# Performance work log

Measured on AMD Instinct MI355X. Metric: run time of the kernel, lower is better.

Reference implementation:

```python
import jax, jax.numpy as jnp
import numpy as np


def setup_inputs() -> dict:
    key = jax.random.key(0)
    k1, k2, k3, k4 = jax.random.split(key, 4)
    B, T, M = 4, 2048, 1024   # batch, seq, d_model -> S = 8192 tokens
    E, F = 16, 4096           # experts (world_size*num_local_experts), d_ff
    x = jax.random.normal(k1, (B, T, M), dtype=jnp.float32) * 0.02
    Wg = jax.random.normal(k2, (M, E), dtype=jnp.float32) * 0.02
    w1 = jax.random.normal(k3, (E, M, F), dtype=jnp.float32) * 0.02
    w2 = jax.random.normal(k4, (E, F, M), dtype=jnp.float32) * 0.02
    return {"x": x, "Wg": Wg, "w1": w1, "w2": w2}


def reference(x, Wg, w1, w2):
    d = x.shape[-1]
    xr = x.reshape(-1, d)                     # (S, M)
    S = xr.shape[0]
    E = Wg.shape[1]
    C = (S + E - 1) // E                      # capacity (capacity_factor = 1.0)

    # top-1 gating (gate module = linear + softmax)
    gate = jax.nn.softmax(xr @ Wg, axis=-1)   # (S, E)
    idx = jnp.argmax(gate, axis=1)            # (S,) expert index per token
    gates_s = jnp.take_along_axis(gate, idx[:, None], axis=1)[:, 0]  # (S,)

    # cumulative-sum location within chosen expert
    onehot = jax.nn.one_hot(idx, E, dtype=jnp.int32)           # (S, E)
    loc = jnp.sum((jnp.cumsum(onehot, axis=0) - 1) * onehot, axis=1)  # (S,)
    valid = loc < C                                             # capacity drop mask

    # scatter dispatch: overflow tokens routed to a pad slot C, then sliced off
    loc_pad = jnp.minimum(loc, C)
    dispatched = jnp.zeros((E, C + 1, d), dtype=x.dtype).at[idx, loc_pad].set(xr)
    dispatched = dispatched[:, :C]            # (E, C, M)

    # all-to-all is identity (FakeAllToAllOp); per-expert FFN
    h = jax.nn.relu(jnp.einsum('ecm,emf->ecf', dispatched, w1))   # (E, C, F)
    expert_out = jnp.einsum('ecf,efm->ecm', h, w2)                # (E, C, M)

    # gather combine: rout[i] = gate_s[i] * expert_out[idx[i], loc[i]] if loc < C
    gathered = expert_out[idx, jnp.minimum(loc, C - 1)]           # (S, M)
    combined = gathered * (gates_s * valid.astype(x.dtype))[:, None]
    return combined.reshape(x.shape)
```

## Files before the change

### kernel.cpp

```cpp
#include <hip/hip_runtime.h>
#include <cstdint>
#include <cstddef>

#define S_TOK 8192
#define DM    1024
#define NE    16
#define NF    4096
#define CAP   512

typedef __attribute__((ext_vector_type(8))) short bf16x8;
typedef __attribute__((ext_vector_type(4))) float f32x4;

__device__ __forceinline__ unsigned short f2bf(float f) {
  __bf16 b = (__bf16)f;
  return __builtin_bit_cast(unsigned short, b);
}
__device__ __forceinline__ unsigned pk2(float a, float b) {
  return (unsigned)f2bf(a) | ((unsigned)f2bf(b) << 16);
}
__device__ __forceinline__ int pcol(int c) { return c ^ ((c >> 3) & 7); }

__device__ __forceinline__ void gload_lds16(const void* g, void* l) {
  __builtin_amdgcn_global_load_lds(
      (const __attribute__((address_space(1))) void*)g,
      (__attribute__((address_space(3))) void*)l, 16, 0, 0);
}

__global__ void __launch_bounds__(256)
zero_kernel(float4* __restrict__ Out, int n4) {
  const int stride = gridDim.x * 256;
  for (int i = blockIdx.x * 256 + threadIdx.x; i < n4; i += stride)
    Out[i] = float4{0.f, 0.f, 0.f, 0.f};
}

__global__ void __launch_bounds__(256)
gate_kernel(const float* __restrict__ X, const float* __restrict__ Wg,
            int* __restrict__ idx, float* __restrict__ gval) {
  const int tid  = threadIdx.x;
  const int lane = tid & 63;
  const int wid  = tid >> 6;
  const int e = lane & 15, q = lane >> 4;
  const int t0 = blockIdx.x * 16 + wid * 4;
  const int mbase = q * 256;

  const float* xp0 = X + (size_t)(t0 + 0) * DM + mbase;
  const float* xp1 = X + (size_t)(t0 + 1) * DM + mbase;
  const float* xp2 = X + (size_t)(t0 + 2) * DM + mbase;
  const float* xp3 = X + (size_t)(t0 + 3) * DM + mbase;
  const float* wp  = Wg + (size_t)mbase * NE + e;

  float a0 = 0.f, a1 = 0.f, a2 = 0.f, a3 = 0.f;
#pragma unroll 4
  for (int i = 0; i < 64; ++i) {
    float4 x0 = *(const float4*)(xp0 + i * 4);
    float4 x1 = *(const float4*)(xp1 + i * 4);
    float4 x2 = *(const float4*)(xp2 + i * 4);
    float4 x3 = *(const float4*)(xp3 + i * 4);
    float w0 = wp[(i * 4 + 0) * NE];
    float w1 = wp[(i * 4 + 1) * NE];
    float w2 = wp[(i * 4 + 2) * NE];
    float w3 = wp[(i * 4 + 3) * NE];
    a0 = fmaf(x0.x, w0, fmaf(x0.y, w1, fmaf(x0.z, w2, fmaf(x0.w, w3, a0))));
    a1 = fmaf(x1.x, w0, fmaf(x1.y, w1, fmaf(x1.z, w2, fmaf(x1.w, w3, a1))));
    a2 = fmaf(x2.x, w0, fmaf(x2.y, w1, fmaf(x2.z, w2, fmaf(x2.w, w3, a2))));
    a3 = fmaf(x3.x, w0, fmaf(x3.y, w1, fmaf(x3.z, w2, fmaf(x3.w, w3, a3))));
  }
#pragma unroll
  for (int s = 16; s < 64; s <<= 1) {
    a0 += __shfl_xor(a0, s, 64);
    a1 += __shfl_xor(a1, s, 64);
    a2 += __shfl_xor(a2, s, 64);
    a3 += __shfl_xor(a3, s, 64);
  }
  float l = (q == 0) ? a0 : (q == 1) ? a1 : (q == 2) ? a2 : a3;
  float bv = l; int bi = e;
#pragma unroll
  for (int s = 1; s < 16; s <<= 1) {
    float ov = __shfl_xor(bv, s, 16);
    int   oi = __shfl_xor(bi, s, 16);
    if (ov > bv || (ov == bv && oi < bi)) { bv = ov; bi = oi; }
  }
  float p  = expf(l - bv);
  float sm = p;
#pragma unroll
  for (int s = 1; s < 16; s <<= 1) sm += __shfl_xor(sm, s, 16);
  if (e == 0) {
    idx[t0 + q]  = bi;
    gval[t0 + q] = 1.0f / sm;
  }
}

__global__ void __launch_bounds__(1024)
scan_kernel(const int* __restrict__ idx, int* __restrict__ s2t) {
  const int tid = threadIdx.x;
#pragma unroll
  for (int k = 0; k < 8; ++k) s2t[tid + k * 1024] = -1;
  __shared__ int base[16];
  __shared__ int wavecnt[16][16];
  if (tid < 16) base[tid] = 0;
  __syncthreads();
  const int wid = tid >> 6, lane = tid & 63;
  const unsigned long long ltmask = (1ull << lane) - 1ull;
  for (int c = 0; c < 8; ++c) {
    const int t = c * 1024 + tid;
    const int e = idx[t];
    int rank = 0;
#pragma unroll
    for (int ee = 0; ee < 16; ++ee) {
      unsigned long long m = __ballot(e == ee);
      if (lane == 0) wavecnt[wid][ee] = __popcll(m);
      if (ee == e) rank = __popcll(m & ltmask);
    }
    __syncthreads();
    if (tid < 16) {
      int s = base[tid];
#pragma unroll
      for (int w = 0; w < 16; ++w) { int cc = wavecnt[w][tid]; wavecnt[w][tid] = s; s += cc; }
      base[tid] = s;
    }
    __syncthreads();
    const int loc = wavecnt[wid][e] + rank;
    if (loc < CAP) s2t[e * CAP + loc] = t;
    __syncthreads();
  }
}

__global__ void __launch_bounds__(256)
gather_kernel(const float* __restrict__ X, const int* __restrict__ s2t,
              unsigned short* __restrict__ Xg) {
  const int tid = threadIdx.x;
  const int d  = tid & 127;
  const int sl = tid >> 7;
  const int s0 = blockIdx.x * 16;
#pragma unroll 2
  for (int p = 0; p < 8; ++p) {
    const int s = s0 + p * 2 + sl;
    const int tok = s2t[s];
    uint4 w;
    if (tok >= 0) {
      const float* xp = X + (size_t)tok * DM + d * 8;
      float4 v0 = *(const float4*)xp;
      float4 v1 = *(const float4*)(xp + 4);
      w = make_uint4(pk2(v0.x, v0.y), pk2(v0.z, v0.w),
                     pk2(v1.x, v1.y), pk2(v1.z, v1.w));
    } else {
      w = make_uint4(0u, 0u, 0u, 0u);
    }
    char* dst = (char*)Xg + (size_t)(s >> 9) * 1048576 +
                (size_t)(d >> 3) * 65536 + (size_t)(d & 7) * 8192 +
                (size_t)(s & 511) * 16;
    *(uint4*)dst = w;
  }
}



#define G1_BX 4
#define G1_BY 32
#define G1_BZ 16
__global__ void __launch_bounds__(256, 2)
gemm1_kernel(const unsigned short* __restrict__ Xg, const float* __restrict__ W1,
             unsigned short* __restrict__ H2) {
  constexpr int NT = DM / 64;
  __shared__ __align__(16) char lds[81920];

  const int tid = threadIdx.x;
  const int lane = tid & 63, wid = tid >> 6;
  const int wr = wid >> 1, wc = wid & 1;
  const int ln15 = lane & 15, l16 = lane >> 4;

  const int flat = blockIdx.x + G1_BX * (blockIdx.y + G1_BY * blockIdx.z);
  const int xcd = flat & 7, jj = flat >> 3;
  const int e  = xcd * 2 + (jj >> 7);
  const int rr = jj & 127;
  const int by = rr >> 2, bx = rr & 3;
  const int m0 = bx * 128, n0 = by * 128;

  char* const Bb0 = lds + 49152;
  char* const Bb1 = lds + 65536;

  const int rb = wid >> 1;
  const int kgw = (wid & 1) * 4;
  const int adst = kgw * 2048 + rb * 1024;
  const char* const Xge = (const char*)Xg + (size_t)e * 1048576 +
                          (size_t)(m0 + rb * 64 + lane) * 16;

  const int c0 = (tid & 31) * 4;
  const int kq = tid >> 5;
  const float* const bsrc = W1 + (size_t)e * DM * NF + (size_t)(kq * 8) * NF + n0 + c0;
  int bwoff[4];
#pragma unroll
  for (int cc = 0; cc < 4; ++cc) bwoff[cc] = kq * 2048 + pcol(c0 + cc) * 16;

  int aoff[4], boff[4];
#pragma unroll
  for (int mi = 0; mi < 4; ++mi)
    aoff[mi] = l16 * 2048 + wr * 1024 + (mi * 16 + ln15) * 16;
#pragma unroll
  for (int ni = 0; ni < 4; ++ni)
    boff[ni] = l16 * 2048 + pcol(wc * 64 + ni * 16 + ln15) * 16;

  f32x4 acc[4][4];
#pragma unroll
  for (int mi = 0; mi < 4; ++mi)
#pragma unroll
    for (int ni = 0; ni < 4; ++ni) acc[mi][ni] = f32x4{0.f, 0.f, 0.f, 0.f};

  float4 breg[8];

  auto ISSUE_B = [&](int kt) {
    const float* bp = bsrc + (size_t)kt * 64 * NF;
#pragma unroll
    for (int r = 0; r < 8; ++r) breg[r] = *(const float4*)(bp + (size_t)r * NF);
  };
  auto ISSUE_A = [&](int Aoff, int kt) {
#pragma unroll
    for (int j = 0; j < 4; ++j)
      gload_lds16(Xge + (size_t)kt * 65536 + (size_t)(kgw + j) * 8192,
                  lds + Aoff + adst + j * 2048);
  };
  auto WRITEB = [&](char* Bbuf) {
    const float* f = (const float*)breg;
#pragma unroll
    for (int cc = 0; cc < 4; ++cc)
      *(uint4*)(Bbuf + bwoff[cc]) =
          make_uint4(pk2(f[0 * 4 + cc], f[1 * 4 + cc]), pk2(f[2 * 4 + cc], f[3 * 4 + cc]),
                     pk2(f[4 * 4 + cc], f[5 * 4 + cc]), pk2(f[6 * 4 + cc], f[7 * 4 + cc]));
  };
  auto COMPUTE = [&](int Aoff, const char* Bbuf) {
#pragma unroll
    for (int kk = 0; kk < 2; ++kk) {
      bf16x8 af[4], bf[4];
#pragma unroll
      for (int mi = 0; mi < 4; ++mi)
        af[mi] = *(const bf16x8*)(lds + Aoff + kk * 8192 + aoff[mi]);
#pragma unroll
      for (int ni = 0; ni < 4; ++ni)
        bf[ni] = *(const bf16x8*)(Bbuf + kk * 8192 + boff[ni]);
#pragma unroll
      for (int mi = 0; mi < 4; ++mi)
#pragma unroll
        for (int ni = 0; ni < 4; ++ni)
          acc[mi][ni] = __builtin_amdgcn_mfma_f32_16x16x32_bf16(af[mi], bf[ni], acc[mi][ni], 0, 0, 0);
    }
  };

  ISSUE_B(0); ISSUE_A(0, 0);
  WRITEB(Bb0);
  ISSUE_B(1); ISSUE_A(16384, 1);
  asm volatile("s_waitcnt vmcnt(12) lgkmcnt(0)" ::: "memory");
  __builtin_amdgcn_s_barrier();

  int aCur = 0, aNxt = 16384, aNx2 = 32768;
  for (int kt = 0; kt < NT; ++kt) {
    WRITEB((kt & 1) ? Bb0 : Bb1);
    const int tl = (kt + 2 < NT) ? kt + 2 : NT - 1;
    ISSUE_B(tl);
    ISSUE_A(aNx2, tl);
    COMPUTE(aCur, (kt & 1) ? Bb1 : Bb0);
    asm volatile("s_waitcnt vmcnt(12) lgkmcnt(0)" ::: "memory");
    __builtin_amdgcn_s_barrier();
    const int t = aCur; aCur = aNxt; aNxt = aNx2; aNx2 = t;
  }
  asm volatile("s_waitcnt vmcnt(0)" ::: "memory");
  __builtin_amdgcn_s_barrier();

  char* img = lds;
#pragma unroll
  for (int mi = 0; mi < 4; ++mi) {
#pragma unroll
    for (int ni = 0; ni < 4; ++ni) {
      const int colL = wc * 64 + ni * 16 + ln15;
      const int basei = (colL >> 6) * 16384 + ((colL >> 3) & 7) * 2048 + (colL & 7) * 2;
#pragma unroll
      for (int j = 0; j < 4; ++j) {
        const int rowL = wr * 64 + mi * 16 + l16 * 4 + j;
        float v = acc[mi][ni][j];
        v = v > 0.f ? v : 0.f;
        *(unsigned short*)(img + basei + rowL * 16) = f2bf(v);
      }
    }
  }
  __syncthreads();
  const char* src = img + tid * 128;
  char* dst = (char*)H2 + (size_t)e * 4194304 +
              (size_t)((n0 >> 6) + (tid >> 7)) * 65536 +
              (size_t)((tid >> 4) & 7) * 8192 +
              (size_t)(m0 + (tid & 15) * 8) * 16;
#pragma unroll
  for (int u = 0; u < 8; ++u)
    *(uint4*)(dst + u * 16) = *(const uint4*)(src + u * 16);
}

#define G2_BX 4
#define G2_BY 8
#define G2_BZ 16
__global__ void __launch_bounds__(256, 2)
gemm2_kernel(const unsigned short* __restrict__ H2, const float* __restrict__ W2,
             const int* __restrict__ s2t, const float* __restrict__ gval,
             float* __restrict__ Out) {
  constexpr int NT = NF / 64;
  __shared__ __align__(16) char lds[81920];

  const int tid = threadIdx.x;
  const int lane = tid & 63, wid = tid >> 6;
  const int wr = wid >> 1, wc = wid & 1;
  const int ln15 = lane & 15, l16 = lane >> 4;

  const int flat = blockIdx.x + G2_BX * (blockIdx.y + G2_BY * blockIdx.z);
  const int xcd = flat & 7, jj = flat >> 3;
  const int e  = xcd * 2 + (jj >> 5);
  const int rr = jj & 31;
  const int by = rr >> 2, bx = rr & 3;
  const int m0 = bx * 128, n0 = by * 128;

  char* const Bb0 = lds + 49152;
  char* const Bb1 = lds + 65536;

  const int rb = wid >> 1;
  const int kgw = (wid & 1) * 4;
  const int adst = kgw * 2048 + rb * 1024;
  const char* const Hex = (const char*)H2 + (size_t)e * 4194304 +
                          (size_t)(m0 + rb * 64 + lane) * 16;

  const int c0 = (tid & 31) * 4;
  const int kq = tid >> 5;
  const float* const bsrc = W2 + (size_t)e * NF * DM + (size_t)(kq * 8) * DM + n0 + c0;
  int bwoff[4];
#pragma unroll
  for (int cc = 0; cc < 4; ++cc) bwoff[cc] = kq * 2048 + pcol(c0 + cc) * 16;

  int aoff[4], boff[4];
#pragma unroll
  for (int mi = 0; mi < 4; ++mi)
    aoff[mi] = l16 * 2048 + wr * 1024 + (mi * 16 + ln15) * 16;
#pragma unroll
  for (int ni = 0; ni < 4; ++ni)
    boff[ni] = l16 * 2048 + pcol(wc * 64 + ni * 16 + ln15) * 16;

  f32x4 acc[4][4];
#pragma unroll
  for (int mi = 0; mi < 4; ++mi)
#pragma unroll
    for (int ni = 0; ni < 4; ++ni) acc[mi][ni] = f32x4{0.f, 0.f, 0.f, 0.f};

  float4 breg[8];

  auto ISSUE_B = [&](int kt) {
    const float* bp = bsrc + (size_t)kt * 64 * DM;
#pragma unroll
    for (int r = 0; r < 8; ++r) breg[r] = *(const float4*)(bp + (size_t)r * DM);
  };
  auto ISSUE_A = [&](int Aoff, int kt) {
#pragma unroll
    for (int j = 0; j < 4; ++j)
      gload_lds16(Hex + (size_t)kt * 65536 + (size_t)(kgw + j) * 8192,
                  lds + Aoff + adst + j * 2048);
  };
  auto WRITEB = [&](char* Bbuf) {
    const float* f = (const float*)breg;
#pragma unroll
    for (int cc = 0; cc < 4; ++cc)
      *(uint4*)(Bbuf + bwoff[cc]) =
          make_uint4(pk2(f[0 * 4 + cc], f[1 * 4 + cc]), pk2(f[2 * 4 + cc], f[3 * 4 + cc]),
                     pk2(f[4 * 4 + cc], f[5 * 4 + cc]), pk2(f[6 * 4 + cc], f[7 * 4 + cc]));
  };
  auto COMPUTE = [&](int Aoff, const char* Bbuf) {
#pragma unroll
    for (int kk = 0; kk < 2; ++kk) {
      bf16x8 af[4], bf[4];
#pragma unroll
      for (int mi = 0; mi < 4; ++mi)
        af[mi] = *(const bf16x8*)(lds + Aoff + kk * 8192 + aoff[mi]);
#pragma unroll
      for (int ni = 0; ni < 4; ++ni)
        bf[ni] = *(const bf16x8*)(Bbuf + kk * 8192 + boff[ni]);
#pragma unroll
      for (int mi = 0; mi < 4; ++mi)
#pragma unroll
        for (int ni = 0; ni < 4; ++ni)
          acc[mi][ni] = __builtin_amdgcn_mfma_f32_16x16x32_bf16(af[mi], bf[ni], acc[mi][ni], 0, 0, 0);
    }
  };

  ISSUE_B(0); ISSUE_A(0, 0);
  WRITEB(Bb0);
  ISSUE_B(1); ISSUE_A(16384, 1);
  asm volatile("s_waitcnt vmcnt(12) lgkmcnt(0)" ::: "memory");
  __builtin_amdgcn_s_barrier();

  int aCur = 0, aNxt = 16384, aNx2 = 32768;
  for (int kt = 0; kt < NT; ++kt) {
    WRITEB((kt & 1) ? Bb0 : Bb1);
    const int tl = (kt + 2 < NT) ? kt + 2 : NT - 1;
    ISSUE_B(tl);
    ISSUE_A(aNx2, tl);
    COMPUTE(aCur, (kt & 1) ? Bb1 : Bb0);
    asm volatile("s_waitcnt vmcnt(12) lgkmcnt(0)" ::: "memory");
    __builtin_amdgcn_s_barrier();
    const int t = aCur; aCur = aNxt; aNxt = aNx2; aNx2 = t;
  }
  asm volatile("s_waitcnt vmcnt(0)" ::: "memory");

#pragma unroll
  for (int mi = 0; mi < 4; ++mi) {
#pragma unroll
    for (int ni = 0; ni < 4; ++ni) {
      const int col = n0 + wc * 64 + ni * 16 + ln15;
#pragma unroll
      for (int j = 0; j < 4; ++j) {
        const int row = m0 + wr * 64 + mi * 16 + l16 * 4 + j;
        const int tk = s2t[e * CAP + row];
        if (tk >= 0)
          Out[(size_t)tk * DM + col] = acc[mi][ni][j] * gval[tk];
      }
    }
  }
}

extern "C" void kernel_launch(void* const* d_in, const int* in_sizes, int n_in,
                              void* d_out, int out_size, void* d_ws, size_t ws_size,
                              hipStream_t stream) {
  (void)in_sizes; (void)n_in; (void)ws_size;
  const float* X  = (const float*)d_in[0];
  const float* Wg = (const float*)d_in[1];
  const float* W1 = (const float*)d_in[2];
  const float* W2 = (const float*)d_in[3];
  float* Out = (float*)d_out;

  char* ws = (char*)d_ws;
  int*   s2t  = (int*)ws;
  int*   idx  = (int*)(ws + 32768);
  float* gval = (float*)(ws + 65536);
  unsigned short* Xg = (unsigned short*)(ws + 98304);
  unsigned short* H2 = (unsigned short*)(ws + 98304 + 16777216);

  zero_kernel<<<2048, 256, 0, stream>>>((float4*)Out, out_size / 4);
  gate_kernel<<<S_TOK / 16, 256, 0, stream>>>(X, Wg, idx, gval);
  scan_kernel<<<1, 1024, 0, stream>>>(idx, s2t);
  gather_kernel<<<512, 256, 0, stream>>>(X, s2t, Xg);
  gemm1_kernel<<<dim3(G1_BX, G1_BY, G1_BZ), 256, 0, stream>>>(Xg, W1, H2);
  gemm2_kernel<<<dim3(G2_BX, G2_BY, G2_BZ), 256, 0, stream>>>(H2, W2, s2t, gval, Out);
}
```

Baseline: 301.2 us.

## Split GEMM tiles across eight waves and deepen B register prefetch

Both expert GEMM kernels move from 256 to 512 threads per block while keeping the 128x128 output tile. Each wave now computes 32x64 instead of 64x64, which halves the accumulators and per-thread global loads and roughly doubles the resident waves per CU to hide memory latency. The B operand is now held in two alternating register buffers, with the loop unrolled by two, so fp32 weight loads are issued one more tile ahead. The cost is more barrier participants, more address overhead per useful MFMA, and lower per-wave operand reuse from LDS.

New measurement: 312.4 us. 3.7% more time.

```diff
diff --git a/kernel.cpp b/kernel.cpp
--- a/kernel.cpp
+++ b/kernel.cpp
@@ -158,7 +158,7 @@
 #define G1_BX 4
 #define G1_BY 32
 #define G1_BZ 16
-__global__ void __launch_bounds__(256, 2)
+__global__ void __launch_bounds__(512, 4)
 gemm1_kernel(const unsigned short* __restrict__ Xg, const float* __restrict__ W1,
              unsigned short* __restrict__ H2) {
   constexpr int NT = DM / 64;
@@ -179,102 +179,109 @@
   char* const Bb0 = lds + 49152;
   char* const Bb1 = lds + 65536;
 
-  const int rb = wid >> 1;
-  const int kgw = (wid & 1) * 4;
-  const int adst = kgw * 2048 + rb * 1024;
-  const char* const Xge = (const char*)Xg + (size_t)e * 1048576 +
-                          (size_t)(m0 + rb * 64 + lane) * 16;
+  const char* const aSrc = (const char*)Xg + (size_t)e * 1048576 +
+                           (size_t)(m0 + (wid & 1) * 64 + lane) * 16;
+  const int adst = (wid >> 1) * 2048 + (wid & 1) * 1024;
 
   const int c0 = (tid & 31) * 4;
   const int kq = tid >> 5;
-  const float* const bsrc = W1 + (size_t)e * DM * NF + (size_t)(kq * 8) * NF + n0 + c0;
+  const float* const bsrc = W1 + (size_t)e * DM * NF + (size_t)(kq * 4) * NF + n0 + c0;
   int bwoff[4];
 #pragma unroll
-  for (int cc = 0; cc < 4; ++cc) bwoff[cc] = kq * 2048 + pcol(c0 + cc) * 16;
-
-  int aoff[4], boff[4];
-#pragma unroll
-  for (int mi = 0; mi < 4; ++mi)
-    aoff[mi] = l16 * 2048 + wr * 1024 + (mi * 16 + ln15) * 16;
+  for (int cc = 0; cc < 4; ++cc)
+    bwoff[cc] = (kq >> 1) * 2048 + pcol(c0 + cc) * 16 + (kq & 1) * 8;
+
+  int aoff[2], boff[4];
+#pragma unroll
+  for (int mi = 0; mi < 2; ++mi)
+    aoff[mi] = l16 * 2048 + (wr * 32 + mi * 16 + ln15) * 16;
 #pragma unroll
   for (int ni = 0; ni < 4; ++ni)
     boff[ni] = l16 * 2048 + pcol(wc * 64 + ni * 16 + ln15) * 16;
 
-  f32x4 acc[4][4];
-#pragma unroll
-  for (int mi = 0; mi < 4; ++mi)
+  f32x4 acc[2][4];
+#pragma unroll
+  for (int mi = 0; mi < 2; ++mi)
 #pragma unroll
     for (int ni = 0; ni < 4; ++ni) acc[mi][ni] = f32x4{0.f, 0.f, 0.f, 0.f};
 
-  float4 breg[8];
-
-  auto ISSUE_B = [&](int kt) {
+  float4 bA[4], bB[4];
+
+  auto ISSUE_B = [&](float4* br, int kt) {
     const float* bp = bsrc + (size_t)kt * 64 * NF;
 #pragma unroll
-    for (int r = 0; r < 8; ++r) breg[r] = *(const float4*)(bp + (size_t)r * NF);
+    for (int r = 0; r < 4; ++r) br[r] = *(const float4*)(bp + (size_t)r * NF);
   };
   auto ISSUE_A = [&](int Aoff, int kt) {
-#pragma unroll
-    for (int j = 0; j < 4; ++j)
-      gload_lds16(Xge + (size_t)kt * 65536 + (size_t)(kgw + j) * 8192,
-                  lds + Aoff + adst + j * 2048);
-  };
-  auto WRITEB = [&](char* Bbuf) {
-    const float* f = (const float*)breg;
+    gload_lds16(aSrc + (size_t)kt * 65536 + (size_t)(wid >> 1) * 8192,
+                lds + Aoff + adst);
+    gload_lds16(aSrc + (size_t)kt * 65536 + (size_t)((wid >> 1) + 4) * 8192,
+                lds + Aoff + adst + 8192);
+  };
+  auto WRITEB = [&](char* Bbuf, const float4* br) {
+    const float* f = (const float*)br;
 #pragma unroll
     for (int cc = 0; cc < 4; ++cc)
-      *(uint4*)(Bbuf + bwoff[cc]) =
-          make_uint4(pk2(f[0 * 4 + cc], f[1 * 4 + cc]), pk2(f[2 * 4 + cc], f[3 * 4 + cc]),
-                     pk2(f[4 * 4 + cc], f[5 * 4 + cc]), pk2(f[6 * 4 + cc], f[7 * 4 + cc]));
+      *(uint2*)(Bbuf + bwoff[cc]) =
+          make_uint2(pk2(f[0 * 4 + cc], f[1 * 4 + cc]),
+                     pk2(f[2 * 4 + cc], f[3 * 4 + cc]));
   };
   auto COMPUTE = [&](int Aoff, const char* Bbuf) {
 #pragma unroll
     for (int kk = 0; kk < 2; ++kk) {
-      bf16x8 af[4], bf[4];
-#pragma unroll
-      for (int mi = 0; mi < 4; ++mi)
+      bf16x8 af[2], bf[4];
+#pragma unroll
+      for (int mi = 0; mi < 2; ++mi)
         af[mi] = *(const bf16x8*)(lds + Aoff + kk * 8192 + aoff[mi]);
 #pragma unroll
       for (int ni = 0; ni < 4; ++ni)
         bf[ni] = *(const bf16x8*)(Bbuf + kk * 8192 + boff[ni]);
 #pragma unroll
-      for (int mi = 0; mi < 4; ++mi)
+      for (int mi = 0; mi < 2; ++mi)
 #pragma unroll
         for (int ni = 0; ni < 4; ++ni)
           acc[mi][ni] = __builtin_amdgcn_mfma_f32_16x16x32_bf16(af[mi], bf[ni], acc[mi][ni], 0, 0, 0);
     }
   };
 
-  ISSUE_B(0); ISSUE_A(0, 0);
-  WRITEB(Bb0);
-  ISSUE_B(1); ISSUE_A(16384, 1);
-  asm volatile("s_waitcnt vmcnt(12) lgkmcnt(0)" ::: "memory");
+  ISSUE_B(bA, 0); ISSUE_A(0, 0);
+  WRITEB(Bb0, bA);
+  ISSUE_B(bB, 1); ISSUE_A(16384, 1);
+  ISSUE_B(bA, 2);
+  asm volatile("s_waitcnt vmcnt(10) lgkmcnt(0)" ::: "memory");
   __builtin_amdgcn_s_barrier();
 
   int aCur = 0, aNxt = 16384, aNx2 = 32768;
-  for (int kt = 0; kt < NT; ++kt) {
-    WRITEB((kt & 1) ? Bb0 : Bb1);
-    const int tl = (kt + 2 < NT) ? kt + 2 : NT - 1;
-    ISSUE_B(tl);
-    ISSUE_A(aNx2, tl);
-    COMPUTE(aCur, (kt & 1) ? Bb1 : Bb0);
-    asm volatile("s_waitcnt vmcnt(12) lgkmcnt(0)" ::: "memory");
+#pragma unroll 1
+  for (int kt = 0; kt < NT; kt += 2) {
+    WRITEB(Bb1, bB);
+    ISSUE_B(bB, (kt + 3 < NT) ? kt + 3 : NT - 1);
+    ISSUE_A(aNx2, (kt + 2 < NT) ? kt + 2 : NT - 1);
+    COMPUTE(aCur, Bb0);
+    asm volatile("s_waitcnt vmcnt(6) lgkmcnt(0)" ::: "memory");
     __builtin_amdgcn_s_barrier();
-    const int t = aCur; aCur = aNxt; aNxt = aNx2; aNx2 = t;
+    int t = aCur; aCur = aNxt; aNxt = aNx2; aNx2 = t;
+    WRITEB(Bb0, bA);
+    ISSUE_B(bA, (kt + 4 < NT) ? kt + 4 : NT - 1);
+    ISSUE_A(aNx2, (kt + 3 < NT) ? kt + 3 : NT - 1);
+    COMPUTE(aCur, Bb1);
+    asm volatile("s_waitcnt vmcnt(6) lgkmcnt(0)" ::: "memory");
+    __builtin_amdgcn_s_barrier();
+    t = aCur; aCur = aNxt; aNxt = aNx2; aNx2 = t;
   }
   asm volatile("s_waitcnt vmcnt(0)" ::: "memory");
   __builtin_amdgcn_s_barrier();
 
   char* img = lds;
 #pragma unroll
-  for (int mi = 0; mi < 4; ++mi) {
+  for (int mi = 0; mi < 2; ++mi) {
 #pragma unroll
     for (int ni = 0; ni < 4; ++ni) {
       const int colL = wc * 64 + ni * 16 + ln15;
       const int basei = (colL >> 6) * 16384 + ((colL >> 3) & 7) * 2048 + (colL & 7) * 2;
 #pragma unroll
       for (int j = 0; j < 4; ++j) {
-        const int rowL = wr * 64 + mi * 16 + l16 * 4 + j;
+        const int rowL = wr * 32 + mi * 16 + l16 * 4 + j;
         float v = acc[mi][ni][j];
         v = v > 0.f ? v : 0.f;
         *(unsigned short*)(img + basei + rowL * 16) = f2bf(v);
@@ -282,20 +289,20 @@
     }
   }
   __syncthreads();
-  const char* src = img + tid * 128;
+  const char* src = img + tid * 64;
   char* dst = (char*)H2 + (size_t)e * 4194304 +
-              (size_t)((n0 >> 6) + (tid >> 7)) * 65536 +
-              (size_t)((tid >> 4) & 7) * 8192 +
-              (size_t)(m0 + (tid & 15) * 8) * 16;
-#pragma unroll
-  for (int u = 0; u < 8; ++u)
+              (size_t)((n0 >> 6) + (tid >> 8)) * 65536 +
+              (size_t)((tid >> 5) & 7) * 8192 +
+              (size_t)(m0 + ((tid * 4) & 127)) * 16;
+#pragma unroll
+  for (int u = 0; u < 4; ++u)
     *(uint4*)(dst + u * 16) = *(const uint4*)(src + u * 16);
 }
 
 #define G2_BX 4
 #define G2_BY 8
 #define G2_BZ 16
-__global__ void __launch_bounds__(256, 2)
+__global__ void __launch_bounds__(512, 4)
 gemm2_kernel(const unsigned short* __restrict__ H2, const float* __restrict__ W2,
              const int* __restrict__ s2t, const float* __restrict__ gval,
              float* __restrict__ Out) {
@@ -317,99 +324,106 @@
   char* const Bb0 = lds + 49152;
   char* const Bb1 = lds + 65536;
 
-  const int rb = wid >> 1;
-  const int kgw = (wid & 1) * 4;
-  const int adst = kgw * 2048 + rb * 1024;
-  const char* const Hex = (const char*)H2 + (size_t)e * 4194304 +
-                          (size_t)(m0 + rb * 64 + lane) * 16;
+  const char* const aSrc = (const char*)H2 + (size_t)e * 4194304 +
+                           (size_t)(m0 + (wid & 1) * 64 + lane) * 16;
+  const int adst = (wid >> 1) * 2048 + (wid & 1) * 1024;
 
   const int c0 = (tid & 31) * 4;
   const int kq = tid >> 5;
-  const float* const bsrc = W2 + (size_t)e * NF * DM + (size_t)(kq * 8) * DM + n0 + c0;
+  const float* const bsrc = W2 + (size_t)e * NF * DM + (size_t)(kq * 4) * DM + n0 + c0;
   int bwoff[4];
 #pragma unroll
-  for (int cc = 0; cc < 4; ++cc) bwoff[cc] = kq * 2048 + pcol(c0 + cc) * 16;
-
-  int aoff[4], boff[4];
-#pragma unroll
-  for (int mi = 0; mi < 4; ++mi)
-    aoff[mi] = l16 * 2048 + wr * 1024 + (mi * 16 + ln15) * 16;
+  for (int cc = 0; cc < 4; ++cc)
+    bwoff[cc] = (kq >> 1) * 2048 + pcol(c0 + cc) * 16 + (kq & 1) * 8;
+
+  int aoff[2], boff[4];
+#pragma unroll
+  for (int mi = 0; mi < 2; ++mi)
+    aoff[mi] = l16 * 2048 + (wr * 32 + mi * 16 + ln15) * 16;
 #pragma unroll
   for (int ni = 0; ni < 4; ++ni)
     boff[ni] = l16 * 2048 + pcol(wc * 64 + ni * 16 + ln15) * 16;
 
-  f32x4 acc[4][4];
-#pragma unroll
-  for (int mi = 0; mi < 4; ++mi)
+  f32x4 acc[2][4];
+#pragma unroll
+  for (int mi = 0; mi < 2; ++mi)
 #pragma unroll
     for (int ni = 0; ni < 4; ++ni) acc[mi][ni] = f32x4{0.f, 0.f, 0.f, 0.f};
 
-  float4 breg[8];
-
-  auto ISSUE_B = [&](int kt) {
+  float4 bA[4], bB[4];
+
+  auto ISSUE_B = [&](float4* br, int kt) {
     const float* bp = bsrc + (size_t)kt * 64 * DM;
 #pragma unroll
-    for (int r = 0; r < 8; ++r) breg[r] = *(const float4*)(bp + (size_t)r * DM);
+    for (int r = 0; r < 4; ++r) br[r] = *(const float4*)(bp + (size_t)r * DM);
   };
   auto ISSUE_A = [&](int Aoff, int kt) {
-#pragma unroll
-    for (int j = 0; j < 4; ++j)
-      gload_lds16(Hex + (size_t)kt * 65536 + (size_t)(kgw + j) * 8192,
-                  lds + Aoff + adst + j * 2048);
-  };
-  auto WRITEB = [&](char* Bbuf) {
-    const float* f = (const float*)breg;
+    gload_lds16(aSrc + (size_t)kt * 65536 + (size_t)(wid >> 1) * 8192,
+                lds + Aoff + adst);
+    gload_lds16(aSrc + (size_t)kt * 65536 + (size_t)((wid >> 1) + 4) * 8192,
+                lds + Aoff + adst + 8192);
+  };
+  auto WRITEB = [&](char* Bbuf, const float4* br) {
+    const float* f = (const float*)br;
 #pragma unroll
     for (int cc = 0; cc < 4; ++cc)
-      *(uint4*)(Bbuf + bwoff[cc]) =
-          make_uint4(pk2(f[0 * 4 + cc], f[1 * 4 + cc]), pk2(f[2 * 4 + cc], f[3 * 4 + cc]),
-                     pk2(f[4 * 4 + cc], f[5 * 4 + cc]), pk2(f[6 * 4 + cc], f[7 * 4 + cc]));
+      *(uint2*)(Bbuf + bwoff[cc]) =
+          make_uint2(pk2(f[0 * 4 + cc], f[1 * 4 + cc]),
+                     pk2(f[2 * 4 + cc], f[3 * 4 + cc]));
   };
   auto COMPUTE = [&](int Aoff, const char* Bbuf) {
 #pragma unroll
     for (int kk = 0; kk < 2; ++kk) {
-      bf16x8 af[4], bf[4];
-#pragma unroll
-      for (int mi = 0; mi < 4; ++mi)
+      bf16x8 af[2], bf[4];
+#pragma unroll
+      for (int mi = 0; mi < 2; ++mi)
         af[mi] = *(const bf16x8*)(lds + Aoff + kk * 8192 + aoff[mi]);
 #pragma unroll
       for (int ni = 0; ni < 4; ++ni)
         bf[ni] = *(const bf16x8*)(Bbuf + kk * 8192 + boff[ni]);
 #pragma unroll
-      for (int mi = 0; mi < 4; ++mi)
+      for (int mi = 0; mi < 2; ++mi)
 #pragma unroll
         for (int ni = 0; ni < 4; ++ni)
           acc[mi][ni] = __builtin_amdgcn_mfma_f32_16x16x32_bf16(af[mi], bf[ni], acc[mi][ni], 0, 0, 0);
     }
   };
 
-  ISSUE_B(0); ISSUE_A(0, 0);
-  WRITEB(Bb0);
-  ISSUE_B(1); ISSUE_A(16384, 1);
-  asm volatile("s_waitcnt vmcnt(12) lgkmcnt(0)" ::: "memory");
+  ISSUE_B(bA, 0); ISSUE_A(0, 0);
+  WRITEB(Bb0, bA);
+  ISSUE_B(bB, 1); ISSUE_A(16384, 1);
+  ISSUE_B(bA, 2);
+  asm volatile("s_waitcnt vmcnt(10) lgkmcnt(0)" ::: "memory");
   __builtin_amdgcn_s_barrier();
 
   int aCur = 0, aNxt = 16384, aNx2 = 32768;
-  for (int kt = 0; kt < NT; ++kt) {
-    WRITEB((kt & 1) ? Bb0 : Bb1);
-    const int tl = (kt + 2 < NT) ? kt + 2 : NT - 1;
-    ISSUE_B(tl);
-    ISSUE_A(aNx2, tl);
-    COMPUTE(aCur, (kt & 1) ? Bb1 : Bb0);
-    asm volatile("s_waitcnt vmcnt(12) lgkmcnt(0)" ::: "memory");
+#pragma unroll 1
+  for (int kt = 0; kt < NT; kt += 2) {
+    WRITEB(Bb1, bB);
+    ISSUE_B(bB, (kt + 3 < NT) ? kt + 3 : NT - 1);
+    ISSUE_A(aNx2, (kt + 2 < NT) ? kt + 2 : NT - 1);
+    COMPUTE(aCur, Bb0);
+    asm volatile("s_waitcnt vmcnt(6) lgkmcnt(0)" ::: "memory");
     __builtin_amdgcn_s_barrier();
-    const int t = aCur; aCur = aNxt; aNxt = aNx2; aNx2 = t;
+    int t = aCur; aCur = aNxt; aNxt = aNx2; aNx2 = t;
+    WRITEB(Bb0, bA);
+    ISSUE_B(bA, (kt + 4 < NT) ? kt + 4 : NT - 1);
+    ISSUE_A(aNx2, (kt + 3 < NT) ? kt + 3 : NT - 1);
+    COMPUTE(aCur, Bb1);
+    asm volatile("s_waitcnt vmcnt(6) lgkmcnt(0)" ::: "memory");
+    __builtin_amdgcn_s_barrier();
+    t = aCur; aCur = aNxt; aNxt = aNx2; aNx2 = t;
   }
   asm volatile("s_waitcnt vmcnt(0)" ::: "memory");
 
 #pragma unroll
-  for (int mi = 0; mi < 4; ++mi) {
+  for (int mi = 0; mi < 2; ++mi) {
 #pragma unroll
     for (int ni = 0; ni < 4; ++ni) {
       const int col = n0 + wc * 64 + ni * 16 + ln15;
 #pragma unroll
       for (int j = 0; j < 4; ++j) {
-        const int row = m0 + wr * 64 + mi * 16 + l16 * 4 + j;
+        const int row = m0 + wr * 32 + mi * 16 + l16 * 4 + j;
         const int tk = s2t[e * CAP + row];
         if (tk >= 0)
           Out[(size_t)tk * DM + col] = acc[mi][ni][j] * gval[tk];
@@ -439,6 +453,6 @@
   gate_kernel<<<S_TOK / 16, 256, 0, stream>>>(X, Wg, idx, gval);
   scan_kernel<<<1, 1024, 0, stream>>>(idx, s2t);
   gather_kernel<<<512, 256, 0, stream>>>(X, s2t, Xg);
-  gemm1_kernel<<<dim3(G1_BX, G1_BY, G1_BZ), 256, 0, stream>>>(Xg, W1, H2);
-  gemm2_kernel<<<dim3(G2_BX, G2_BY, G2_BZ), 256, 0, stream>>>(H2, W2, s2t, gval, Out);
-}
+  gemm1_kernel<<<dim3(G1_BX, G1_BY, G1_BZ), 512, 0, stream>>>(Xg, W1, H2);
+  gemm2_kernel<<<dim3(G2_BX, G2_BY, G2_BZ), 512, 0, stream>>>(H2, W2, s2t, gval, Out);
+}
```

## Restructure GEMM pipelines with register double-buffered B and smaller LDS for occupancy

Applied to the files above, without the earlier changes.

Both expert GEMM kernels drop from 80KB to 48KB of LDS. They now use a single B tile in LDS and double-buffer the fp32 B loads in registers (bP/bQ), with two A buffers alternated in an unrolled-by-2 loop. Launch bounds rise to 3 blocks per CU, and MFMA sections are wrapped in s_setprio to favour matrix issue. The extra register buffer and the added barriers per iteration may raise register pressure and cause spills at the higher occupancy target. Wrapped (kt+N)&NTM prefetches issue redundant loads at the tail.

After: 1.001 ms. 3.32x slower.

```diff
diff --git a/kernel.cpp b/kernel.cpp
--- a/kernel.cpp
+++ b/kernel.cpp
@@ -158,11 +158,12 @@
 #define G1_BX 4
 #define G1_BY 32
 #define G1_BZ 16
-__global__ void __launch_bounds__(256, 2)
+__global__ void __launch_bounds__(256, 3)
 gemm1_kernel(const unsigned short* __restrict__ Xg, const float* __restrict__ W1,
              unsigned short* __restrict__ H2) {
   constexpr int NT = DM / 64;
-  __shared__ __align__(16) char lds[81920];
+  constexpr int NTM = NT - 1;
+  __shared__ __align__(16) char lds[49152];
 
   const int tid = threadIdx.x;
   const int lane = tid & 63, wid = tid >> 6;
@@ -176,29 +177,28 @@
   const int by = rr >> 2, bx = rr & 3;
   const int m0 = bx * 128, n0 = by * 128;
 
-  char* const Bb0 = lds + 49152;
-  char* const Bb1 = lds + 65536;
+  char* const Bs = lds + 32768;
 
   const int rb = wid >> 1;
   const int kgw = (wid & 1) * 4;
   const int adst = kgw * 2048 + rb * 1024;
-  const char* const Xge = (const char*)Xg + (size_t)e * 1048576 +
-                          (size_t)(m0 + rb * 64 + lane) * 16;
+  const char* const aSrc = (const char*)Xg + (size_t)e * 1048576 +
+                           (size_t)(m0 + rb * 64 + lane) * 16;
 
   const int c0 = (tid & 31) * 4;
   const int kq = tid >> 5;
   const float* const bsrc = W1 + (size_t)e * DM * NF + (size_t)(kq * 8) * NF + n0 + c0;
   int bwoff[4];
 #pragma unroll
-  for (int cc = 0; cc < 4; ++cc) bwoff[cc] = kq * 2048 + pcol(c0 + cc) * 16;
+  for (int cc = 0; cc < 4; ++cc) bwoff[cc] = 32768 + kq * 2048 + pcol(c0 + cc) * 16;
 
   int aoff[4], boff[4];
 #pragma unroll
   for (int mi = 0; mi < 4; ++mi)
-    aoff[mi] = l16 * 2048 + wr * 1024 + (mi * 16 + ln15) * 16;
+    aoff[mi] = l16 * 2048 + (wr * 64 + mi * 16 + ln15) * 16;
 #pragma unroll
   for (int ni = 0; ni < 4; ++ni)
-    boff[ni] = l16 * 2048 + pcol(wc * 64 + ni * 16 + ln15) * 16;
+    boff[ni] = 32768 + l16 * 2048 + pcol(wc * 64 + ni * 16 + ln15) * 16;
 
   f32x4 acc[4][4];
 #pragma unroll
@@ -206,28 +206,28 @@
 #pragma unroll
     for (int ni = 0; ni < 4; ++ni) acc[mi][ni] = f32x4{0.f, 0.f, 0.f, 0.f};
 
-  float4 breg[8];
-
-  auto ISSUE_B = [&](int kt) {
+  float4 bP[8], bQ[8];
+
+  auto ISSUE_B = [&](float4* br, int kt) {
     const float* bp = bsrc + (size_t)kt * 64 * NF;
 #pragma unroll
-    for (int r = 0; r < 8; ++r) breg[r] = *(const float4*)(bp + (size_t)r * NF);
+    for (int r = 0; r < 8; ++r) br[r] = *(const float4*)(bp + (size_t)r * NF);
   };
   auto ISSUE_A = [&](int Aoff, int kt) {
 #pragma unroll
     for (int j = 0; j < 4; ++j)
-      gload_lds16(Xge + (size_t)kt * 65536 + (size_t)(kgw + j) * 8192,
+      gload_lds16(aSrc + (size_t)kt * 65536 + (size_t)(kgw + j) * 8192,
                   lds + Aoff + adst + j * 2048);
   };
-  auto WRITEB = [&](char* Bbuf) {
-    const float* f = (const float*)breg;
+  auto WRITEB = [&](const float4* br) {
+    const float* f = (const float*)br;
 #pragma unroll
     for (int cc = 0; cc < 4; ++cc)
-      *(uint4*)(Bbuf + bwoff[cc]) =
+      *(uint4*)(lds + bwoff[cc]) =
           make_uint4(pk2(f[0 * 4 + cc], f[1 * 4 + cc]), pk2(f[2 * 4 + cc], f[3 * 4 + cc]),
                      pk2(f[4 * 4 + cc], f[5 * 4 + cc]), pk2(f[6 * 4 + cc], f[7 * 4 + cc]));
   };
-  auto COMPUTE = [&](int Aoff, const char* Bbuf) {
+  auto COMPUTE = [&](int Aoff) {
 #pragma unroll
     for (int kk = 0; kk < 2; ++kk) {
       bf16x8 af[4], bf[4];
@@ -236,31 +236,40 @@
         af[mi] = *(const bf16x8*)(lds + Aoff + kk * 8192 + aoff[mi]);
 #pragma unroll
       for (int ni = 0; ni < 4; ++ni)
-        bf[ni] = *(const bf16x8*)(Bbuf + kk * 8192 + boff[ni]);
+        bf[ni] = *(const bf16x8*)(lds + kk * 8192 + boff[ni]);
+      __builtin_amdgcn_s_setprio(1);
 #pragma unroll
       for (int mi = 0; mi < 4; ++mi)
 #pragma unroll
         for (int ni = 0; ni < 4; ++ni)
           acc[mi][ni] = __builtin_amdgcn_mfma_f32_16x16x32_bf16(af[mi], bf[ni], acc[mi][ni], 0, 0, 0);
-    }
-  };
-
-  ISSUE_B(0); ISSUE_A(0, 0);
-  WRITEB(Bb0);
-  ISSUE_B(1); ISSUE_A(16384, 1);
-  asm volatile("s_waitcnt vmcnt(12) lgkmcnt(0)" ::: "memory");
+      __builtin_amdgcn_s_setprio(0);
+    }
+  };
+
+  ISSUE_B(bP, 0);  ISSUE_A(0, 0);
+  ISSUE_B(bQ, 1);  ISSUE_A(16384, 1);
+  WRITEB(bP);
+  ISSUE_B(bP, 2);
+  asm volatile("s_waitcnt vmcnt(20) lgkmcnt(0)" ::: "memory");
   __builtin_amdgcn_s_barrier();
 
-  int aCur = 0, aNxt = 16384, aNx2 = 32768;
-  for (int kt = 0; kt < NT; ++kt) {
-    WRITEB((kt & 1) ? Bb0 : Bb1);
-    const int tl = (kt + 2 < NT) ? kt + 2 : NT - 1;
-    ISSUE_B(tl);
-    ISSUE_A(aNx2, tl);
-    COMPUTE(aCur, (kt & 1) ? Bb1 : Bb0);
+#pragma unroll 1
+  for (int kt = 0; kt < NT; kt += 2) {
+    COMPUTE(0);
+    __builtin_amdgcn_s_barrier();
+    WRITEB(bQ);
+    ISSUE_B(bQ, (kt + 3) & NTM);
+    ISSUE_A(0, (kt + 2) & NTM);
     asm volatile("s_waitcnt vmcnt(12) lgkmcnt(0)" ::: "memory");
     __builtin_amdgcn_s_barrier();
-    const int t = aCur; aCur = aNxt; aNxt = aNx2; aNx2 = t;
+    COMPUTE(16384);
+    __builtin_amdgcn_s_barrier();
+    WRITEB(bP);
+    ISSUE_B(bP, (kt + 4) & NTM);
+    ISSUE_A(16384, (kt + 3) & NTM);
+    asm volatile("s_waitcnt vmcnt(12) lgkmcnt(0)" ::: "memory");
+    __builtin_amdgcn_s_barrier();
   }
   asm volatile("s_waitcnt vmcnt(0)" ::: "memory");
   __builtin_amdgcn_s_barrier();
@@ -295,12 +304,13 @@
 #define G2_BX 4
 #define G2_BY 8
 #define G2_BZ 16
-__global__ void __launch_bounds__(256, 2)
+__global__ void __launch_bounds__(256, 3)
 gemm2_kernel(const unsigned short* __restrict__ H2, const float* __restrict__ W2,
              const int* __restrict__ s2t, const float* __restrict__ gval,
              float* __restrict__ Out) {
   constexpr int NT = NF / 64;
-  __shared__ __align__(16) char lds[81920];
+  constexpr int NTM = NT - 1;
+  __shared__ __align__(16) char lds[49152];
 
   const int tid = threadIdx.x;
   const int lane = tid & 63, wid = tid >> 6;
@@ -314,29 +324,26 @@
   const int by = rr >> 2, bx = rr & 3;
   const int m0 = bx * 128, n0 = by * 128;
 
-  char* const Bb0 = lds + 49152;
-  char* const Bb1 = lds + 65536;
-
   const int rb = wid >> 1;
   const int kgw = (wid & 1) * 4;
   const int adst = kgw * 2048 + rb * 1024;
-  const char* const Hex = (const char*)H2 + (size_t)e * 4194304 +
-                          (size_t)(m0 + rb * 64 + lane) * 16;
+  const char* const aSrc = (const char*)H2 + (size_t)e * 4194304 +
+                           (size_t)(m0 + rb * 64 + lane) * 16;
 
   const int c0 = (tid & 31) * 4;
   const int kq = tid >> 5;
   const float* const bsrc = W2 + (size_t)e * NF * DM + (size_t)(kq * 8) * DM + n0 + c0;
   int bwoff[4];
 #pragma unroll
-  for (int cc = 0; cc < 4; ++cc) bwoff[cc] = kq * 2048 + pcol(c0 + cc) * 16;
+  for (int cc = 0; cc < 4; ++cc) bwoff[cc] = 32768 + kq * 2048 + pcol(c0 + cc) * 16;
 
   int aoff[4], boff[4];
 #pragma unroll
   for (int mi = 0; mi < 4; ++mi)
-    aoff[mi] = l16 * 2048 + wr * 1024 + (mi * 16 + ln15) * 16;
+    aoff[mi] = l16 * 2048 + (wr * 64 + mi * 16 + ln15) * 16;
 #pragma unroll
   for (int ni = 0; ni < 4; ++ni)
-    boff[ni] = l16 * 2048 + pcol(wc * 64 + ni * 16 + ln15) * 16;
+    boff[ni] = 32768 + l16 * 2048 + pcol(wc * 64 + ni * 16 + ln15) * 16;
 
   f32x4 acc[4][4];
 #pragma unroll
@@ -344,28 +351,28 @@
 #pragma unroll
     for (int ni = 0; ni < 4; ++ni) acc[mi][ni] = f32x4{0.f, 0.f, 0.f, 0.f};
 
-  float4 breg[8];
-
-  auto ISSUE_B = [&](int kt) {
+  float4 bP[8], bQ[8];
+
+  auto ISSUE_B = [&](float4* br, int kt) {
     const float* bp = bsrc + (size_t)kt * 64 * DM;
 #pragma unroll
-    for (int r = 0; r < 8; ++r) breg[r] = *(const float4*)(bp + (size_t)r * DM);
+    for (int r = 0; r < 8; ++r) br[r] = *(const float4*)(bp + (size_t)r * DM);
   };
   auto ISSUE_A = [&](int Aoff, int kt) {
 #pragma unroll
     for (int j = 0; j < 4; ++j)
-      gload_lds16(Hex + (size_t)kt * 65536 + (size_t)(kgw + j) * 8192,
+      gload_lds16(aSrc + (size_t)kt * 65536 + (size_t)(kgw + j) * 8192,
                   lds + Aoff + adst + j * 2048);
   };
-  auto WRITEB = [&](char* Bbuf) {
-    const float* f = (const float*)breg;
+  auto WRITEB = [&](const float4* br) {
+    const float* f = (const float*)br;
 #pragma unroll
     for (int cc = 0; cc < 4; ++cc)
-      *(uint4*)(Bbuf + bwoff[cc]) =
+      *(uint4*)(lds + bwoff[cc]) =
           make_uint4(pk2(f[0 * 4 + cc], f[1 * 4 + cc]), pk2(f[2 * 4 + cc], f[3 * 4 + cc]),
                      pk2(f[4 * 4 + cc], f[5 * 4 + cc]), pk2(f[6 * 4 + cc], f[7 * 4 + cc]));
   };
-  auto COMPUTE = [&](int Aoff, const char* Bbuf) {
+  auto COMPUTE = [&](int Aoff) {
 #pragma unroll
     for (int kk = 0; kk < 2; ++kk) {
       bf16x8 af[4], bf[4];
@@ -374,31 +381,40 @@
         af[mi] = *(const bf16x8*)(lds + Aoff + kk * 8192 + aoff[mi]);
 #pragma unroll
       for (int ni = 0; ni < 4; ++ni)
-        bf[ni] = *(const bf16x8*)(Bbuf + kk * 8192 + boff[ni]);
+        bf[ni] = *(const bf16x8*)(lds + kk * 8192 + boff[ni]);
+      __builtin_amdgcn_s_setprio(1);
 #pragma unroll
       for (int mi = 0; mi < 4; ++mi)
 #pragma unroll
         for (int ni = 0; ni < 4; ++ni)
           acc[mi][ni] = __builtin_amdgcn_mfma_f32_16x16x32_bf16(af[mi], bf[ni], acc[mi][ni], 0, 0, 0);
-    }
-  };
-
-  ISSUE_B(0); ISSUE_A(0, 0);
-  WRITEB(Bb0);
-  ISSUE_B(1); ISSUE_A(16384, 1);
-  asm volatile("s_waitcnt vmcnt(12) lgkmcnt(0)" ::: "memory");
+      __builtin_amdgcn_s_setprio(0);
+    }
+  };
+
+  ISSUE_B(bP, 0);  ISSUE_A(0, 0);
+  ISSUE_B(bQ, 1);  ISSUE_A(16384, 1);
+  WRITEB(bP);
+  ISSUE_B(bP, 2);
+  asm volatile("s_waitcnt vmcnt(20) lgkmcnt(0)" ::: "memory");
   __builtin_amdgcn_s_barrier();
 
-  int aCur = 0, aNxt = 16384, aNx2 = 32768;
-  for (int kt = 0; kt < NT; ++kt) {
-    WRITEB((kt & 1) ? Bb0 : Bb1);
-    const int tl = (kt + 2 < NT) ? kt + 2 : NT - 1;
-    ISSUE_B(tl);
-    ISSUE_A(aNx2, tl);
-    COMPUTE(aCur, (kt & 1) ? Bb1 : Bb0);
+#pragma unroll 1
+  for (int kt = 0; kt < NT; kt += 2) {
+    COMPUTE(0);
+    __builtin_amdgcn_s_barrier();
+    WRITEB(bQ);
+    ISSUE_B(bQ, (kt + 3) & NTM);
+    ISSUE_A(0, (kt + 2) & NTM);
     asm volatile("s_waitcnt vmcnt(12) lgkmcnt(0)" ::: "memory");
     __builtin_amdgcn_s_barrier();
-    const int t = aCur; aCur = aNxt; aNxt = aNx2; aNx2 = t;
+    COMPUTE(16384);
+    __builtin_amdgcn_s_barrier();
+    WRITEB(bP);
+    ISSUE_B(bP, (kt + 4) & NTM);
+    ISSUE_A(16384, (kt + 3) & NTM);
+    asm volatile("s_waitcnt vmcnt(12) lgkmcnt(0)" ::: "memory");
+    __builtin_amdgcn_s_barrier();
   }
   asm volatile("s_waitcnt vmcnt(0)" ::: "memory");
 
```
